# Optimization experiments

Measured on AMD Instinct MI355X. Metric: run time of the kernel, lower is better.

Reference implementation:

```python
import jax, jax.numpy as jnp
import numpy as np


def setup_inputs() -> dict:
    key = jax.random.key(0)
    k0, k1, k2, k3, k4 = jax.random.split(key, 5)
    B, NODE, FRAME = 16, 25, 128
    x = jax.random.normal(k0, (B, NODE, FRAME), dtype=jnp.float32)
    # 1x1 convs with in_dim = out_dim = 1 reduce to scalar weight + bias
    w1 = jax.random.normal(k1, (), dtype=jnp.float32)
    b1 = jax.random.normal(k2, (), dtype=jnp.float32)
    w2 = jax.random.normal(k3, (), dtype=jnp.float32)
    b2 = jax.random.normal(k4, (), dtype=jnp.float32)
    return {"x": x, "w1": w1, "b1": b1, "w2": w2, "b2": b2}


def reference(x, w1, b1, w2, b2):
    B, node_num, frame = x.shape
    N = node_num * frame
    xf = x.reshape(B, 1, N)                 # [B, 1, N] (C=1)
    dep_1 = (w1 * xf + b1).transpose(0, 2, 1)   # [B, N, 1]
    dep_2 = w2 * xf + b2                        # [B, 1, N]
    dep = jnp.einsum('bnc,bcm->bnm', dep_1, dep_2)  # [B, N, N] rank-1 scores
    impli_dep = jax.nn.softmax(dep, axis=-1)
    # bmm(proj_data [B,1,N], impli_dep^T [B,N,N]) -> [B,1,N]
    out = jnp.einsum('bcn,bmn->bcm', xf, impli_dep)
    out = out.reshape(B, 1, node_num, frame)
    return out + x.reshape(B, 1, node_num, frame)
```

## Files before the change

kernel.cpp:

```cpp
#include <hip/hip_runtime.h>
#include <math.h>


#define BATCH 16
#define NTOT  3200
#define N4    (NTOT / 4)
#define K     256
#define KBLOCKS 32
#define KPB   (K / KBLOCKS)
#define SUBW  32
#define BLOCK 256
#define LOG2E 1.44269504088896340736f

__device__ inline float fast_exp2(float v) {
#if __has_builtin(__builtin_amdgcn_exp2f)
    return __builtin_amdgcn_exp2f(v);
#else
    return exp2f(v);
#endif
}

__global__ __launch_bounds__(BLOCK) void table_kernel(
    const float* __restrict__ x,
    const float* __restrict__ w1p, const float* __restrict__ b1p,
    const float* __restrict__ w2p,
    float* __restrict__ table, float2* __restrict__ params)
{
    __shared__ float4 xs4[N4];
    __shared__ float red[8];

    const int bid = blockIdx.x;
    const int b   = bid >> 5;
    const int kb  = bid & (KBLOCKS - 1);
    const int t   = threadIdx.x;

    const float w1 = *w1p, b1 = *b1p, w2 = *w2p;
    const float c1 = w1 * w2, c0 = b1 * w2;

    const float4* xb4 = (const float4*)(x + b * NTOT);
    float mx = -INFINITY, mn = INFINITY;
    for (int i = t; i < N4; i += BLOCK) {
        float4 v = xb4[i];
        xs4[i] = v;
        mx = fmaxf(fmaxf(mx, v.x), fmaxf(v.y, fmaxf(v.z, v.w)));
        mn = fminf(fminf(mn, v.x), fminf(v.y, fminf(v.z, v.w)));
    }
    #pragma unroll
    for (int off = 1; off < 64; off <<= 1) {
        mx = fmaxf(mx, __shfl_xor(mx, off));
        mn = fminf(mn, __shfl_xor(mn, off));
    }
    const int wid = t >> 6;
    if ((t & 63) == 0) { red[wid] = mx; red[4 + wid] = mn; }
    __syncthreads();
    const float xmax = fmaxf(fmaxf(red[0], red[1]), fmaxf(red[2], red[3]));
    const float xmin = fminf(fminf(red[4], red[5]), fminf(red[6], red[7]));

    const float tmin  = (c1 >= 0.f) ? fmaf(c1, xmin, c0) : fmaf(c1, xmax, c0);
    const float tmax  = (c1 >= 0.f) ? fmaf(c1, xmax, c0) : fmaf(c1, xmin, c0);
    const float delta = (tmax - tmin) * (1.0f / (K - 1));

    const int g = t >> 5;
    const int s = t & (SUBW - 1);
    const int k = kb * KPB + g;
    const float tk = fmaf((float)k, delta, tmin);
    const float a2 = tk * LOG2E;
    const float M2 = a2 * ((a2 >= 0.f) ? xmax : xmin);

    float sA = 0.f, sB = 0.f, wA = 0.f, wB = 0.f;
    #pragma unroll 5
    for (int i = 0; i < N4 / SUBW; ++i) {
        float4 v = xs4[s + SUBW * i];
        float e0 = fast_exp2(fmaf(a2, v.x, -M2));
        float e1 = fast_exp2(fmaf(a2, v.y, -M2));
        float e2 = fast_exp2(fmaf(a2, v.z, -M2));
        float e3 = fast_exp2(fmaf(a2, v.w, -M2));
        sA += e0 + e1;  sB += e2 + e3;
        wA = fmaf(v.x, e0, wA);  wA = fmaf(v.y, e1, wA);
        wB = fmaf(v.z, e2, wB);  wB = fmaf(v.w, e3, wB);
    }
    float sum = sA + sB, ws = wA + wB;
    #pragma unroll
    for (int off = 1; off < SUBW; off <<= 1) {
        sum += __shfl_xor(sum, off);
        ws  += __shfl_xor(ws,  off);
    }
    if (s == 0) table[b * K + k] = ws / sum;
    if (kb == 0 && t == 0)
        params[b] = make_float2(tmin, delta != 0.f ? 1.0f / delta : 0.f);
}

__global__ __launch_bounds__(BLOCK) void apply_kernel(
    const float* __restrict__ x,
    const float* __restrict__ w1p, const float* __restrict__ b1p,
    const float* __restrict__ w2p,
    const float* __restrict__ table, const float2* __restrict__ params,
    float* __restrict__ out)
{
    const int gid4 = blockIdx.x * BLOCK + threadIdx.x;
    const int b    = gid4 / (N4);
    const float c1 = (*w1p) * (*w2p), c0 = (*b1p) * (*w2p);
    const float2 pr = params[b];
    const float* tb = table + b * K;

    float4 xv = ((const float4*)x)[gid4];
    float4 ov;
    #pragma unroll
    for (int j = 0; j < 4; ++j) {
        float xm = (&xv.x)[j];
        float u = (fmaf(c1, xm, c0) - pr.x) * pr.y;
        u = fminf(fmaxf(u, 0.f), (float)(K - 1));
        int i = min((int)u, K - 2);
        float frac = u - (float)i;
        float lo = tb[i], hi = tb[i + 1];
        (&ov.x)[j] = fmaf(frac, hi - lo, lo) + xm;
    }
    ((float4*)out)[gid4] = ov;
}

extern "C" void kernel_launch(void* const* d_in, const int* in_sizes, int n_in,
                              void* d_out, int out_size, void* d_ws, size_t ws_size,
                              hipStream_t stream) {
    const float* x  = (const float*)d_in[0];
    const float* w1 = (const float*)d_in[1];
    const float* b1 = (const float*)d_in[2];
    const float* w2 = (const float*)d_in[3];
    const float* b2 = (const float*)d_in[4];
    (void)b2;
    float* out = (float*)d_out;

    float*  table  = (float*)d_ws;
    float2* params = (float2*)((char*)d_ws + BATCH * K * sizeof(float));

    table_kernel<<<BATCH * KBLOCKS, BLOCK, 0, stream>>>(x, w1, b1, w2, table, params);
    apply_kernel<<<(BATCH * NTOT) / (BLOCK * 4), BLOCK, 0, stream>>>(
        x, w1, b1, w2, table, params, out);
}
```

Measured before the change: 11.80 us.

## Fuse table build and interpolation into one kernel with per-block table slices

Merges the table-building and apply kernels into a single launch. Each of 1024 blocks computes 4 table entries plus one boundary entry redundantly, keeps them in shared memory, then scans the whole batch row and writes only the outputs whose interpolation interval falls in its slice. This removes the second launch and the global table round-trip. In exchange each block rescans all 3200 elements and does scattered, divergent scalar stores, and boundary entries are computed twice across blocks.

```diff
diff --git a/kernel.cpp b/kernel.cpp
--- a/kernel.cpp
+++ b/kernel.cpp
@@ -6,10 +6,10 @@
 #define NTOT  3200
 #define N4    (NTOT / 4)
 #define K     256
-#define KBLOCKS 32
-#define KPB   (K / KBLOCKS)
-#define SUBW  32
+#define QB    64
+#define KPB   (K / QB)
 #define BLOCK 256
+#define GRID  (BATCH * QB)
 #define LOG2E 1.44269504088896340736f
 
 __device__ inline float fast_exp2(float v) {
@@ -20,22 +20,24 @@
 #endif
 }
 
-__global__ __launch_bounds__(BLOCK) void table_kernel(
+__global__ __launch_bounds__(BLOCK) void fused1_kernel(
     const float* __restrict__ x,
     const float* __restrict__ w1p, const float* __restrict__ b1p,
     const float* __restrict__ w2p,
-    float* __restrict__ table, float2* __restrict__ params)
+    float* __restrict__ out)
 {
     __shared__ float4 xs4[N4];
     __shared__ float red[8];
+    __shared__ float red2[8];
+    __shared__ float lt[KPB + 1];
 
     const int bid = blockIdx.x;
-    const int b   = bid >> 5;
-    const int kb  = bid & (KBLOCKS - 1);
+    const int b   = bid >> 6;
+    const int q   = bid & (QB - 1);
     const int t   = threadIdx.x;
 
-    const float w1 = *w1p, b1 = *b1p, w2 = *w2p;
-    const float c1 = w1 * w2, c0 = b1 * w2;
+    const float c1 = (*w1p) * (*w2p);
+    const float c0 = (*b1p) * (*w2p);
 
     const float4* xb4 = (const float4*)(x + b * NTOT);
     float mx = -INFINITY, mn = INFINITY;
@@ -59,63 +61,79 @@
     const float tmin  = (c1 >= 0.f) ? fmaf(c1, xmin, c0) : fmaf(c1, xmax, c0);
     const float tmax  = (c1 >= 0.f) ? fmaf(c1, xmax, c0) : fmaf(c1, xmin, c0);
     const float delta = (tmax - tmin) * (1.0f / (K - 1));
+    const float inv   = (delta != 0.f) ? 1.0f / delta : 0.f;
 
-    const int g = t >> 5;
-    const int s = t & (SUBW - 1);
-    const int k = kb * KPB + g;
-    const float tk = fmaf((float)k, delta, tmin);
-    const float a2 = tk * LOG2E;
-    const float M2 = a2 * ((a2 >= 0.f) ? xmax : xmin);
+    const int g = t >> 6;
+    const int s = t & 63;
+    {
+        const float tk = fmaf((float)(q * KPB + g), delta, tmin);
+        const float a2 = tk * LOG2E;
+        const float M2 = a2 * ((a2 >= 0.f) ? xmax : xmin);
+        float sum = 0.f, ws = 0.f;
+        for (int i = s; i < N4; i += 64) {
+            float4 v = xs4[i];
+            float e0 = fast_exp2(fmaf(a2, v.x, -M2));
+            float e1 = fast_exp2(fmaf(a2, v.y, -M2));
+            float e2 = fast_exp2(fmaf(a2, v.z, -M2));
+            float e3 = fast_exp2(fmaf(a2, v.w, -M2));
+            sum += (e0 + e1) + (e2 + e3);
+            ws = fmaf(v.x, e0, ws); ws = fmaf(v.y, e1, ws);
+            ws = fmaf(v.z, e2, ws); ws = fmaf(v.w, e3, ws);
+        }
+        #pragma unroll
+        for (int off = 1; off < 64; off <<= 1) {
+            sum += __shfl_xor(sum, off);
+            ws  += __shfl_xor(ws,  off);
+        }
+        if (s == 0) lt[g] = ws / sum;
+    }
 
-    float sA = 0.f, sB = 0.f, wA = 0.f, wB = 0.f;
-    #pragma unroll 5
-    for (int i = 0; i < N4 / SUBW; ++i) {
-        float4 v = xs4[s + SUBW * i];
-        float e0 = fast_exp2(fmaf(a2, v.x, -M2));
-        float e1 = fast_exp2(fmaf(a2, v.y, -M2));
-        float e2 = fast_exp2(fmaf(a2, v.z, -M2));
-        float e3 = fast_exp2(fmaf(a2, v.w, -M2));
-        sA += e0 + e1;  sB += e2 + e3;
-        wA = fmaf(v.x, e0, wA);  wA = fmaf(v.y, e1, wA);
-        wB = fmaf(v.z, e2, wB);  wB = fmaf(v.w, e3, wB);
+    {
+        const float tk = fmaf((float)(q * KPB + KPB), delta, tmin);
+        const float a2 = tk * LOG2E;
+        const float M2 = a2 * ((a2 >= 0.f) ? xmax : xmin);
+        float sum = 0.f, ws = 0.f;
+        for (int i = t; i < N4; i += BLOCK) {
+            float4 v = xs4[i];
+            float e0 = fast_exp2(fmaf(a2, v.x, -M2));
+            float e1 = fast_exp2(fmaf(a2, v.y, -M2));
+            float e2 = fast_exp2(fmaf(a2, v.z, -M2));
+            float e3 = fast_exp2(fmaf(a2, v.w, -M2));
+            sum += (e0 + e1) + (e2 + e3);
+            ws = fmaf(v.x, e0, ws); ws = fmaf(v.y, e1, ws);
+            ws = fmaf(v.z, e2, ws); ws = fmaf(v.w, e3, ws);
+        }
+        #pragma unroll
+        for (int off = 1; off < 64; off <<= 1) {
+            sum += __shfl_xor(sum, off);
+            ws  += __shfl_xor(ws,  off);
+        }
+        if ((t & 63) == 0) { red2[wid] = sum; red2[4 + wid] = ws; }
+        __syncthreads();
+        if (t == 0) {
+            float S = ((red2[0] + red2[1]) + (red2[2] + red2[3]));
+            float W = ((red2[4] + red2[5]) + (red2[6] + red2[7]));
+            lt[KPB] = W / S;
+        }
+        __syncthreads();
     }
-    float sum = sA + sB, ws = wA + wB;
-    #pragma unroll
-    for (int off = 1; off < SUBW; off <<= 1) {
-        sum += __shfl_xor(sum, off);
-        ws  += __shfl_xor(ws,  off);
+
+    for (int i = t; i < N4; i += BLOCK) {
+        float4 xv = xs4[i];
+        #pragma unroll
+        for (int j = 0; j < 4; ++j) {
+            float xm = (&xv.x)[j];
+            float u = (fmaf(c1, xm, c0) - tmin) * inv;
+            u = fminf(fmaxf(u, 0.f), (float)(K - 1));
+            int ii = min((int)u, K - 2);
+            if ((ii >> 2) == q) {
+                float frac = u - (float)ii;
+                int   li   = ii - q * KPB;
+                float lo = lt[li], hi = lt[li + 1];
+                out[b * NTOT + i * 4 + j] = fmaf(frac, hi - lo, lo) + xm;
+            }
+        }
     }
-    if (s == 0) table[b * K + k] = ws / sum;
-    if (kb == 0 && t == 0)
-        params[b] = make_float2(tmin, delta != 0.f ? 1.0f / delta : 0.f);
-}
-
-__global__ __launch_bounds__(BLOCK) void apply_kernel(
-    const float* __restrict__ x,
-    const float* __restrict__ w1p, const float* __restrict__ b1p,
-    const float* __restrict__ w2p,
-    const float* __restrict__ table, const float2* __restrict__ params,
-    float* __restrict__ out)
-{
-    const int gid4 = blockIdx.x * BLOCK + threadIdx.x;
-    const int b    = gid4 / (N4);
-    const float c1 = (*w1p) * (*w2p), c0 = (*b1p) * (*w2p);
-    const float2 pr = params[b];
-    const float* tb = table + b * K;
-
-    float4 xv = ((const float4*)x)[gid4];
-    float4 ov;
-    #pragma unroll
-    for (int j = 0; j < 4; ++j) {
-        float xm = (&xv.x)[j];
-        float u = (fmaf(c1, xm, c0) - pr.x) * pr.y;
-        u = fminf(fmaxf(u, 0.f), (float)(K - 1));
-        int i = min((int)u, K - 2);
-        float frac = u - (float)i;
-        float lo = tb[i], hi = tb[i + 1];
-        (&ov.x)[j] = fmaf(frac, hi - lo, lo) + xm;
-    }
-    ((float4*)out)[gid4] = ov;
 }
 
 extern "C" void kernel_launch(void* const* d_in, const int* in_sizes, int n_in,
@@ -129,10 +147,5 @@
     (void)b2;
     float* out = (float*)d_out;
 
-    float*  table  = (float*)d_ws;
-    float2* params = (float2*)((char*)d_ws + BATCH * K * sizeof(float));
-
-    table_kernel<<<BATCH * KBLOCKS, BLOCK, 0, stream>>>(x, w1, b1, w2, table, params);
-    apply_kernel<<<(BATCH * NTOT) / (BLOCK * 4), BLOCK, 0, stream>>>(
-        x, w1, b1, w2, table, params, out);
+    fused1_kernel<<<dim3(GRID), dim3(BLOCK), 0, stream>>>(x, w1, b1, w2, out);
 }
```

Result: slower. 13.51 us (+14.5%).
